# Performance work log

Measured on AMD Instinct MI355X. Metric: run time of the kernel, lower is better.

Reference implementation:

```python
import jax, jax.numpy as jnp
import numpy as np

N = 100000
E = 1600000
F_IN = 128
NHID = 50
NOUT = 50


def gcn_conv(x, W, b, src, dst, n):
    # x: [N, Fin] -> transform first (PyG GCNConv order)
    h = x @ W  # [N, Fout]
    # symmetric normalization with self-loops already included in src/dst
    ones = jnp.ones(src.shape[0], dtype=h.dtype)
    deg = jax.ops.segment_sum(ones, dst, num_segments=n)  # in-degree incl self-loop
    dinv = jnp.where(deg > 0, jax.lax.rsqrt(deg), 0.0)
    norm = dinv[src] * dinv[dst]  # [E']
    msgs = h[src] * norm[:, None]  # gather + scale, [E', Fout]
    out = jax.ops.segment_sum(msgs, dst, num_segments=n)  # scatter-add
    return out + b


def setup_inputs() -> dict:
    key = jax.random.key(0)
    k1, k2, k3, k4, k5, k6 = jax.random.split(key, 6)
    x = jax.random.normal(k1, (N, F_IN), dtype=jnp.float32)
    edge_index = jax.random.randint(k2, (2, E), 0, N, dtype=jnp.int64) if jax.config.read('jax_enable_x64') else jax.random.randint(k2, (2, E), 0, N, dtype=jnp.int32)
    # Glorot-ish init for weights
    W1 = jax.random.normal(k3, (F_IN, NHID), dtype=jnp.float32) * (1.0 / np.sqrt(F_IN))
    b1 = jnp.zeros((NHID,), dtype=jnp.float32)
    W2 = jax.random.normal(k4, (NHID, NOUT), dtype=jnp.float32) * (1.0 / np.sqrt(NHID))
    b2 = jnp.zeros((NOUT,), dtype=jnp.float32)
    return {"x": x, "W1": W1, "b1": b1, "W2": W2, "b2": b2, "edge_index": edge_index}


def reference(x, W1, b1, W2, b2, edge_index):
    n = x.shape[0]
    # add self-loops once (shared by both layers)
    loop = jnp.arange(n, dtype=edge_index.dtype)
    src = jnp.concatenate([edge_index[0], loop])
    dst = jnp.concatenate([edge_index[1], loop])
    h = gcn_conv(x, W1, b1, src, dst, n)
    h = jax.nn.relu(h)
    # dropout is identity in eval mode (training=False)
    out = gcn_conv(h, W2, b2, src, dst, n)
    return out
```

## Files before the change

kernel.cpp:

```cpp
#include <hip/hip_runtime.h>
#include <hip/hip_fp16.h>

#define FIN 128
#define FH 50
#define HSTRIDE 64
#define MAXNB 1024
#define BSHIFT 7
#define BSIZE 128
#define CAP 3072
#define PCHUNK 4096
#define SRCMASK 0x01FFFFFFu


__global__ __launch_bounds__(256) void partition_kernel(const int* __restrict__ src,
                                                        const int* __restrict__ dst,
                                                        int* __restrict__ gcursor,
                                                        unsigned int* __restrict__ packed,
                                                        int E, int NB) {
    __shared__ int hist[MAXNB];
    __shared__ int wbase[MAXNB];
    int t = threadIdx.x;
    int base = blockIdx.x * PCHUNK;
    for (int i = t; i < NB; i += 256) hist[i] = 0;
    __syncthreads();
#pragma unroll 4
    for (int i = 0; i < PCHUNK / 256; i++) {
        int e = base + t + i * 256;
        if (e < E) atomicAdd(&hist[dst[e] >> BSHIFT], 1);
    }
    __syncthreads();
    for (int i = t; i < NB; i += 256) {
        int c = hist[i];
        wbase[i] = c ? atomicAdd(&gcursor[i], c) : 0;
        hist[i] = 0;
    }
    __syncthreads();
#pragma unroll 4
    for (int i = 0; i < PCHUNK / 256; i++) {
        int e = base + t + i * 256;
        if (e < E) {
            unsigned int s = (unsigned int)src[e];
            int d = dst[e];
            int b = d >> BSHIFT;
            int off = atomicAdd(&hist[b], 1);
            packed[(size_t)b * CAP + wbase[b] + off] =
                ((unsigned int)(d & (BSIZE - 1)) << 25) | s;
        }
    }
}

__global__ __launch_bounds__(256) void bucket_build_kernel(const unsigned int* __restrict__ packed,
                                                           const int* __restrict__ gcursor,
                                                           int* __restrict__ rbeg,
                                                           int* __restrict__ rend,
                                                           float* __restrict__ dinv,
                                                           int* __restrict__ csr, int n) {
    __shared__ int degl[BSIZE];
    __shared__ int excl[BSIZE];
    __shared__ int lcur[BSIZE];
    int b = blockIdx.x;
    int t = threadIdx.x;
    int nbeg = b << BSHIFT;
    int sbase = b * CAP;
    int cnt = gcursor[b];
    if (t < BSIZE) degl[t] = 0;
    __syncthreads();
    for (int e = t; e < cnt; e += 256)
        atomicAdd(&degl[packed[sbase + e] >> 25], 1);
    __syncthreads();
    int v = (t < BSIZE) ? degl[t] : 0;
    if (t < BSIZE) excl[t] = v;
    __syncthreads();
    for (int off = 1; off < BSIZE; off <<= 1) {
        int add = (t >= off && t < BSIZE) ? excl[t - off] : 0;
        __syncthreads();
        if (t < BSIZE) excl[t] += add;
        __syncthreads();
    }
    if (t < BSIZE) {
        int ex = excl[t] - v;
        int node = nbeg + t;
        if (node < n) {
            rbeg[node] = sbase + ex;
            rend[node] = sbase + ex + v;
            dinv[node] = rsqrtf((float)v + 1.0f);
        }
        lcur[t] = ex;
    }
    __syncthreads();
    for (int e = t; e < cnt; e += 256) {
        unsigned int w = packed[sbase + e];
        int off = atomicAdd(&lcur[w >> 25], 1);
        csr[sbase + off] = (int)(w & SRCMASK);
    }
}


__global__ __launch_bounds__(256) void gemm1_kernel(
    const float* __restrict__ x, const float* __restrict__ W,
    const float* __restrict__ dinv, __half* __restrict__ hs1,
    __half* __restrict__ hs2, int n) {
    __shared__ float Ws[FIN * FH];
    int t = threadIdx.x;
    for (int i = t; i < FIN * FH; i += 256) Ws[i] = W[i];
    if (blockIdx.x == 0) {
        if (t < HSTRIDE)           hs1[((size_t)n << 6) + t] = __float2half(0.f);
        else if (t < 2 * HSTRIDE)  hs2[((size_t)n << 6) + (t - HSTRIDE)] = __float2half(0.f);
    }
    __syncthreads();
    int row = blockIdx.x * 128 + (t >> 1);
    int kh = t & 1;
    if (row >= n) return;
    float a[FH];
#pragma unroll
    for (int c = 0; c < FH; c++) a[c] = 0.f;
    const float4* xr = (const float4*)(x + (size_t)row * FIN + kh * 64);
#pragma unroll
    for (int k4 = 0; k4 < 16; k4++) {
        float4 xv = xr[k4];
        const float* w0 = &Ws[(kh * 64 + k4 * 4) * FH];
#pragma unroll
        for (int c = 0; c < FH; c++) {
            a[c] = fmaf(xv.x, w0[c], a[c]);
            a[c] = fmaf(xv.y, w0[c + FH], a[c]);
            a[c] = fmaf(xv.z, w0[c + 2 * FH], a[c]);
            a[c] = fmaf(xv.w, w0[c + 3 * FH], a[c]);
        }
    }
#pragma unroll
    for (int c = 0; c < FH; c++) a[c] += __shfl_xor(a[c], 1);
    if (kh == 0) {
        float dv = dinv[row];
        __half2* hp = (__half2*)(hs1 + ((size_t)row << 6));
#pragma unroll
        for (int c = 0; c < HSTRIDE / 2; c++) {
            float lo = (2 * c     < FH) ? a[2 * c] * dv     : 0.f;
            float hi = (2 * c + 1 < FH) ? a[2 * c + 1] * dv : 0.f;
            hp[c] = __floats2half2_rn(lo, hi);
        }
    }
}

__global__ __launch_bounds__(256) void gemm2_kernel(
    const float* __restrict__ h1, const float* __restrict__ W,
    const float* __restrict__ dinv, __half* __restrict__ hs2, int n) {
    __shared__ float Ws[FH * FH];
    int t = threadIdx.x;
    for (int i = t; i < FH * FH; i += 256) Ws[i] = W[i];
    __syncthreads();
    int row = blockIdx.x * 64 + (t >> 2);
    int q = t & 3;
    if (row >= n) return;
    int c0 = q ? (12 * q + 2) : 0;
    const float* xp = h1 + (size_t)row * FH;
    float xr[FH];
#pragma unroll
    for (int k = 0; k < FH; k++) xr[k] = xp[k];
    float a[14];
#pragma unroll
    for (int c = 0; c < 14; c++) a[c] = 0.f;
    for (int k = 0; k < FH; k++) {
        float xv = xr[k];
        const float* w = &Ws[k * FH + c0];
#pragma unroll
        for (int c = 0; c < 14; c++) a[c] = fmaf(xv, w[c], a[c]);
    }
    float dv = dinv[row];
    __half2* hp = (__half2*)(hs2 + ((size_t)row << 6) + c0);
    int nst = q ? 6 : 7;
    for (int j = 0; j < nst; j++)
        hp[j] = __floats2half2_rn(a[2 * j] * dv, a[2 * j + 1] * dv);
}

__global__ __launch_bounds__(256) void gather_kernel(
    const __half* __restrict__ hs, const int* __restrict__ rbeg,
    const int* __restrict__ rend, const int* __restrict__ csr,
    const float* __restrict__ dinv, const float* __restrict__ b,
    float* __restrict__ out, int n, int do_relu) {
    int wid = blockIdx.x * 4 + (threadIdx.x >> 6);
    int lane = threadIdx.x & 63;
    if (wid >= n) return;
    int beg = rbeg[wid];
    int end = rend[wid];
    float acc = __half2float(hs[((size_t)wid << 6) + lane]);
    for (int base = beg; base < end; base += 64) {
        int rem = end - base;
        int idx = (lane < rem) ? csr[base + lane] : n;
        int cnt = rem < 64 ? rem : 64;
        for (int j = 0; j < cnt; j += 16) {
            float v[16];
#pragma unroll
            for (int u = 0; u < 16; u++) {
                int s = __shfl(idx, j + u);
                v[u] = __half2float(hs[((size_t)s << 6) + lane]);
            }
            float s01 = (v[0] + v[1]) + (v[2] + v[3]);
            float s23 = (v[4] + v[5]) + (v[6] + v[7]);
            float s45 = (v[8] + v[9]) + (v[10] + v[11]);
            float s67 = (v[12] + v[13]) + (v[14] + v[15]);
            acc += (s01 + s23) + (s45 + s67);
        }
    }
    if (lane < FH) {
        float o = fmaf(dinv[wid], acc, b[lane]);
        if (do_relu) o = fmaxf(o, 0.f);
        out[(size_t)wid * FH + lane] = o;
    }
}

extern "C" void kernel_launch(void* const* d_in, const int* in_sizes, int n_in,
                              void* d_out, int out_size, void* d_ws, size_t ws_size,
                              hipStream_t stream) {
    const float* x  = (const float*)d_in[0];
    const float* W1 = (const float*)d_in[1];
    const float* b1 = (const float*)d_in[2];
    const float* W2 = (const float*)d_in[3];
    const float* b2 = (const float*)d_in[4];
    const int*   ei = (const int*)d_in[5];

    int n = in_sizes[0] / FIN;
    int E = in_sizes[5] / 2;
    const int* src = ei;
    const int* dst = ei + E;
    int NB = (n + BSIZE - 1) >> BSHIFT;

    char* ws = (char*)d_ws;
    size_t off = 0;
    auto alloc = [&](size_t bytes) {
        void* p = ws + off;
        off = (off + bytes + 511) & ~(size_t)511;
        return p;
    };
    size_t hs_bytes   = (size_t)(n + 1) * HSTRIDE * 2;
    size_t slab_bytes = (size_t)NB * CAP * 4;
    size_t un_bytes   = slab_bytes > hs_bytes ? slab_bytes : hs_bytes;

    int*          gcursor = (int*)alloc((size_t)MAXNB * 4);
    int*          rbeg    = (int*)alloc((size_t)n * 4);
    int*          rend    = (int*)alloc((size_t)n * 4);
    float*        dinv    = (float*)alloc((size_t)n * 4);
    int*          csr     = (int*)alloc(slab_bytes);
    __half*       hs1     = (__half*)alloc(hs_bytes);
    void*         un      = alloc(un_bytes);
    unsigned int* packed  = (unsigned int*)un;
    __half*       hs2     = (__half*)un;
    float*        out     = (float*)d_out;

    hipMemsetAsync(gcursor, 0, (size_t)MAXNB * 4, stream);

    int pChunks = (E + PCHUNK - 1) / PCHUNK;
    partition_kernel<<<pChunks, 256, 0, stream>>>(src, dst, gcursor, packed, E, NB);
    bucket_build_kernel<<<NB, 256, 0, stream>>>(packed, gcursor, rbeg, rend, dinv, csr, n);

    int g1Blocks = (n + 127) / 128;
    int g2Blocks = (n + 63) / 64;
    int gatherBlocks = (n + 3) / 4;

    gemm1_kernel<<<g1Blocks, 256, 0, stream>>>(x, W1, dinv, hs1, hs2, n);
    gather_kernel<<<gatherBlocks, 256, 0, stream>>>(hs1, rbeg, rend, csr, dinv, b1, out, n, 1);
    gemm2_kernel<<<g2Blocks, 256, 0, stream>>>(out, W2, dinv, hs2, n);
    gather_kernel<<<gatherBlocks, 256, 0, stream>>>(hs2, rbeg, rend, csr, dinv, b2, out, n, 0);
}
```

Measured before the change: 288.0 us.

## Transpose and pad weight tiles in LDS for float4 reads in both GEMMs

Both small GEMM kernels now store W transposed in shared memory (output-column major, padded row stride), so each thread reads a float4 of four k values per output column instead of four scalar loads. gemm1 pads the k dimension per half to avoid bank conflicts. gemm2 is remapped from 4 threads per row with 14 columns each to 2 threads per row with 26 columns each, with a float2 tail for k=48..49. The goal is fewer LDS instructions per FMA; the trade-off is more accumulator registers in gemm2 and half as many threads per row.

```diff
diff --git a/kernel.cpp b/kernel.cpp
--- a/kernel.cpp
+++ b/kernel.cpp
@@ -96,13 +96,18 @@
 }
 
 
+#define W1S 136
 __global__ __launch_bounds__(256) void gemm1_kernel(
     const float* __restrict__ x, const float* __restrict__ W,
     const float* __restrict__ dinv, __half* __restrict__ hs1,
     __half* __restrict__ hs2, int n) {
-    __shared__ float Ws[FIN * FH];
-    int t = threadIdx.x;
-    for (int i = t; i < FIN * FH; i += 256) Ws[i] = W[i];
+    __shared__ __align__(16) float Ws[FH * W1S];
+    int t = threadIdx.x;
+    for (int i = t; i < FIN * FH; i += 256) {
+        int k = i / FH;
+        int c = i - k * FH;
+        Ws[c * W1S + k + ((k >> 6) << 2)] = W[i];
+    }
     if (blockIdx.x == 0) {
         if (t < HSTRIDE)           hs1[((size_t)n << 6) + t] = __float2half(0.f);
         else if (t < 2 * HSTRIDE)  hs2[((size_t)n << 6) + (t - HSTRIDE)] = __float2half(0.f);
@@ -115,16 +120,16 @@
 #pragma unroll
     for (int c = 0; c < FH; c++) a[c] = 0.f;
     const float4* xr = (const float4*)(x + (size_t)row * FIN + kh * 64);
-#pragma unroll
+    const float4* W4 = (const float4*)Ws;
+    int wbase = kh * 17;
     for (int k4 = 0; k4 < 16; k4++) {
         float4 xv = xr[k4];
-        const float* w0 = &Ws[(kh * 64 + k4 * 4) * FH];
+        const float4* wk = W4 + wbase + k4;
 #pragma unroll
         for (int c = 0; c < FH; c++) {
-            a[c] = fmaf(xv.x, w0[c], a[c]);
-            a[c] = fmaf(xv.y, w0[c + FH], a[c]);
-            a[c] = fmaf(xv.z, w0[c + 2 * FH], a[c]);
-            a[c] = fmaf(xv.w, w0[c + 3 * FH], a[c]);
+            float4 wv = wk[c * 34];
+            a[c] = fmaf(xv.w, wv.w, fmaf(xv.z, wv.z,
+                   fmaf(xv.y, wv.y, fmaf(xv.x, wv.x, a[c]))));
         }
     }
 #pragma unroll
@@ -141,33 +146,48 @@
     }
 }
 
+#define W2S 13
 __global__ __launch_bounds__(256) void gemm2_kernel(
     const float* __restrict__ h1, const float* __restrict__ W,
     const float* __restrict__ dinv, __half* __restrict__ hs2, int n) {
-    __shared__ float Ws[FH * FH];
-    int t = threadIdx.x;
-    for (int i = t; i < FH * FH; i += 256) Ws[i] = W[i];
-    __syncthreads();
-    int row = blockIdx.x * 64 + (t >> 2);
-    int q = t & 3;
+    __shared__ __align__(16) float Ws[52 * 52];
+    int t = threadIdx.x;
+    for (int i = t; i < FH * FH; i += 256) {
+        int k = i / FH;
+        int c = i - k * FH;
+        Ws[c * 52 + k] = W[i];
+    }
+    for (int i = t; i < 2 * 52; i += 256) Ws[FH * 52 + i] = 0.f;
+    __syncthreads();
+    int row = blockIdx.x * 128 + (t >> 1);
+    int ch = t & 1;
     if (row >= n) return;
-    int c0 = q ? (12 * q + 2) : 0;
     const float* xp = h1 + (size_t)row * FH;
     float xr[FH];
 #pragma unroll
     for (int k = 0; k < FH; k++) xr[k] = xp[k];
-    float a[14];
-#pragma unroll
-    for (int c = 0; c < 14; c++) a[c] = 0.f;
-    for (int k = 0; k < FH; k++) {
-        float xv = xr[k];
-        const float* w = &Ws[k * FH + c0];
-#pragma unroll
-        for (int c = 0; c < 14; c++) a[c] = fmaf(xv, w[c], a[c]);
+    float a[26];
+#pragma unroll
+    for (int c = 0; c < 26; c++) a[c] = 0.f;
+    const float4* W4 = (const float4*)Ws;
+    int cbase = ch * 26;
+    for (int k4 = 0; k4 < 12; k4++) {
+#pragma unroll
+        for (int c = 0; c < 26; c++) {
+            float4 wv = W4[(cbase + c) * W2S + k4];
+            a[c] = fmaf(xr[4 * k4 + 3], wv.w, fmaf(xr[4 * k4 + 2], wv.z,
+                   fmaf(xr[4 * k4 + 1], wv.y, fmaf(xr[4 * k4], wv.x, a[c]))));
+        }
+    }
+    const float2* W2v = (const float2*)Ws;
+#pragma unroll
+    for (int c = 0; c < 26; c++) {
+        float2 wt = W2v[(cbase + c) * 26 + 24];
+        a[c] = fmaf(xr[49], wt.y, fmaf(xr[48], wt.x, a[c]));
     }
     float dv = dinv[row];
-    __half2* hp = (__half2*)(hs2 + ((size_t)row << 6) + c0);
-    int nst = q ? 6 : 7;
+    __half2* hp = (__half2*)(hs2 + ((size_t)row << 6) + cbase);
+    int nst = ch ? 12 : 13;
     for (int j = 0; j < nst; j++)
         hp[j] = __floats2half2_rn(a[2 * j] * dv, a[2 * j + 1] * dv);
 }
@@ -253,7 +273,7 @@
     bucket_build_kernel<<<NB, 256, 0, stream>>>(packed, gcursor, rbeg, rend, dinv, csr, n);
 
     int g1Blocks = (n + 127) / 128;
-    int g2Blocks = (n + 63) / 64;
+    int g2Blocks = (n + 127) / 128;
     int gatherBlocks = (n + 3) / 4;
 
     gemm1_kernel<<<g1Blocks, 256, 0, stream>>>(x, W1, dinv, hs1, hs2, n);
```

Result: no change. 284.5 us (-1.2%).
